# Performance work log

Hardware: AMD Instinct MI355X
Metric: run time of the kernel (lower is better)

## Reference

```python
import jax, jax.numpy as jnp
import numpy as np

BATCH = 1024
N_KPS = 24
N_IN = 6
N_HID = 128
N_OUT = 2
N_EDGES = N_KPS * (N_KPS - 1)  # 552, fully-connected minus self-loops
BN_EPS = 1e-5


def _xavier(key, shape):
    # torch xavier_normal_: std = sqrt(2 / (fan_in + fan_out)); Linear weight is [out, in]
    std = np.sqrt(2.0 / (shape[0] + shape[1])).astype(np.float32)
    return jax.random.normal(key, shape, dtype=jnp.float32) * std


def _mlp(x, w1, b1, w2, b2, g, be):
    # Two-layer ELU MLP followed by training-mode BatchNorm1d over flattened (B*N, C)
    h = jax.nn.elu(jnp.einsum('bnd,hd->bnh', x, w1) + b1)
    h = jax.nn.elu(jnp.einsum('bnd,hd->bnh', h, w2) + b2)
    mean = h.mean(axis=(0, 1))
    var = h.var(axis=(0, 1))  # biased variance, as torch BN uses for normalization
    return g * (h - mean) * jax.lax.rsqrt(var + BN_EPS) + be


def setup_inputs() -> dict:
    key = jax.random.key(0)
    ks = jax.random.split(key, 12)
    # structural one-hot receiver/sender matrices for fully-connected graph (no self-loops)
    off = ~np.eye(N_KPS, dtype=bool)
    recv_idx, send_idx = np.nonzero(off)
    eye = np.eye(N_KPS, dtype=np.float32)
    rel_rec = jnp.asarray(eye[recv_idx])    # [E, N]
    rel_send = jnp.asarray(eye[send_idx])   # [E, N]

    inputs = jax.random.normal(ks[0], (BATCH, N_KPS, N_IN), dtype=jnp.float32)

    def mlp_params(k, n_in):
        k1, k2 = jax.random.split(k)
        return dict(
            w1=_xavier(k1, (N_HID, n_in)), b1=jnp.full((N_HID,), 0.1, jnp.float32),
            w2=_xavier(k2, (N_HID, N_HID)), b2=jnp.full((N_HID,), 0.1, jnp.float32),
            g=jnp.ones((N_HID,), jnp.float32), be=jnp.zeros((N_HID,), jnp.float32))

    m1 = mlp_params(ks[1], N_IN)
    m2 = mlp_params(ks[2], 2 * N_HID)
    m3 = mlp_params(ks[3], N_HID)
    m4 = mlp_params(ks[4], 3 * N_HID)
    fo_w = _xavier(ks[5], (N_OUT, N_HID * N_KPS))
    fo_b = jnp.full((N_OUT,), 0.1, jnp.float32)

    d = {'inputs': inputs, 'rel_rec': rel_rec, 'rel_send': rel_send,
         'fo_w': fo_w, 'fo_b': fo_b}
    for name, p in [('m1', m1), ('m2', m2), ('m3', m3), ('m4', m4)]:
        for k2, v in p.items():
            d[f'{name}_{k2}'] = v
    return d


def reference(inputs, rel_rec, rel_send,
              fo_w, fo_b,
              m1_w1, m1_b1, m1_w2, m1_b2, m1_g, m1_be,
              m2_w1, m2_b1, m2_w2, m2_b2, m2_g, m2_be,
              m3_w1, m3_b1, m3_w2, m3_b2, m3_g, m3_be,
              m4_w1, m4_b1, m4_w2, m4_b2, m4_g, m4_be):
    B, N = inputs.shape[0], inputs.shape[1]
    x = inputs.reshape(B, N, -1)

    def node2edge(x):  # [B,N,C] -> [B,E,2C]
        recv = jnp.einsum('en,bnc->bec', rel_rec, x)
        send = jnp.einsum('en,bnc->bec', rel_send, x)
        return jnp.concatenate([recv, send], axis=2)

    def edge2node(x):  # [B,E,C] -> [B,N,C], averaged by N (= incoming.size(1))
        return jnp.einsum('en,bec->bnc', rel_rec, x) / N

    x = _mlp(x, m1_w1, m1_b1, m1_w2, m1_b2, m1_g, m1_be)            # [B,N,H]
    x = _mlp(node2edge(x), m2_w1, m2_b1, m2_w2, m2_b2, m2_g, m2_be)  # [B,E,H]
    x_skip = x
    x = _mlp(edge2node(x), m3_w1, m3_b1, m3_w2, m3_b2, m3_g, m3_be)  # [B,N,H]
    x = node2edge(x)                                                  # [B,E,2H]
    x = jnp.concatenate([x, x_skip], axis=2)                          # [B,E,3H]
    x = _mlp(x, m4_w1, m4_b1, m4_w2, m4_b2, m4_g, m4_be)              # [B,E,H]
    x = edge2node(x)                                                  # [B,N,H]
    x = x.reshape(B, -1)                                              # [B,N*H]
    return x @ fo_w.T + fo_b                                          # [B,n_out]
```

## Files before the change

### kernel.cpp

```cpp
#include <hip/hip_runtime.h>

typedef __bf16 bf16;
typedef __bf16 b16x8 __attribute__((ext_vector_type(8)));
typedef __bf16 b16x4 __attribute__((ext_vector_type(4)));
typedef float f32x4 __attribute__((ext_vector_type(4)));

#define TB 256
#define LDA 136
#define LDI 40
#define NB 1024
#define NK 24
#define NE 552
#define NH 128
#define BEcnt (NB*NE)
#define BNODE (NB*NK)
#define EPS 1e-5f

#define S_BN1 0
#define S_BN3 2048
#define S_A2  4096
#define S_A4  20480
#define S_B41 36864
#define STATS_ZERO_BYTES 147456
#define WB_M1W2 0
#define WB_M2W1 16384
#define WB_M2W2 49152
#define WB_M3W1 65536
#define WB_M3W2 81920
#define WB_M4W1 98304
#define WB_M4W2 147456
#define WB_M4W1S 163840
#define OFF_WBF 150528ull
#define OFF_H1  516096ull
#define OFF_H3  (OFF_H1 + 6291456ull)
#define OFF_Y2R (OFF_H3 + 6291456ull)
#define OFF_Y2S (OFF_Y2R + 6291456ull)
#define OFF_Y4R (OFF_Y2S + 6291456ull)
#define OFF_Y4S (OFF_Y4R + 6291456ull)
#define OFF_Z2  (OFF_Y4S + 6291456ull)
#define OFF_Z4  (OFF_Z2  + 12582912ull)
#define OFF_H2  (OFF_Z4  + 12582912ull)

__device__ __forceinline__ float elu(float x){ return x > 0.f ? x : __expf(x) - 1.f; }

__device__ __forceinline__ void swizzle_bt(int id, int& b, int& tile4){
  int x = id & 7, j = id >> 3;
  int bt = j / 6;
  int tile = j - bt*6;
  b = x*128 + bt;
  tile4 = tile*4;
}

__device__ __forceinline__ void load_bfrags_bf(const bf16* W, int ldw, int k0,
                                               b16x8 bfr[4][2], int lane, int w){
  int n = lane & 15, q = lane >> 4;
  #pragma unroll
  for (int kb=0; kb<4; ++kb)
    #pragma unroll
    for (int t=0; t<2; ++t)
      bfr[kb][t] = *(const b16x8*)(W + (size_t)((w*2+t)*16 + n)*ldw + k0 + kb*32 + q*8);
}

template<int MT>
__device__ __forceinline__ void gemm_regB_t(const bf16* As, const b16x8 bfr[4][2],
                                            f32x4 acc[MT][2], int lane){
  int m = lane & 15, q = lane >> 4;
  #pragma unroll
  for (int kb=0; kb<4; ++kb){
    int ka = kb*32 + q*8;
    b16x8 a[MT];
    #pragma unroll
    for (int mt=0; mt<MT; ++mt)
      a[mt] = *(const b16x8*)(As + (mt*16+m)*LDA + ka);
    #pragma unroll
    for (int mt=0; mt<MT; ++mt)
      #pragma unroll
      for (int t=0; t<2; ++t)
        acc[mt][t] = __builtin_amdgcn_mfma_f32_16x16x32_bf16(a[mt], bfr[kb][t], acc[mt][t], 0,0,0);
  }
}

template<int MT>
__device__ __forceinline__ void zero_acc_t(f32x4 acc[MT][2]){
  #pragma unroll
  for (int mt=0; mt<MT; ++mt)
    #pragma unroll
    for (int t=0; t<2; ++t){ acc[mt][t][0]=0.f; acc[mt][t][1]=0.f; acc[mt][t][2]=0.f; acc[mt][t][3]=0.f; }
}

template<int MT>
__device__ __forceinline__ void epilogue_to_lds_t(const f32x4 acc[MT][2], const float* bias, bf16* As,
                                                  int lane, int w, int validRows){
  int q = lane >> 4, n = lane & 15;
  #pragma unroll
  for (int mt=0; mt<MT; ++mt)
    #pragma unroll
    for (int t=0; t<2; ++t){
      int col = (w*2+t)*16 + n;
      float bc = bias[col];
      #pragma unroll
      for (int i=0; i<4; ++i){
        int row = mt*16 + q*4 + i;
        float v = (row < validRows) ? elu(acc[mt][t][i] + bc) : 0.f;
        As[row*LDA + col] = (bf16)v;
      }
    }
}

template<int MT>
__device__ __forceinline__ void write_acc_bf_t(const f32x4 acc[MT][2], bf16* out, int lane, int w){
  int q = lane >> 4, n = lane & 15;
  #pragma unroll
  for (int mt=0; mt<MT; ++mt)
    #pragma unroll
    for (int t=0; t<2; ++t){
      int col = (w*2+t)*16 + n;
      #pragma unroll
      for (int i=0; i<4; ++i)
        out[(size_t)(mt*16 + q*4 + i)*NH + col] = (bf16)acc[mt][t][i];
    }
}

__device__ __forceinline__ void store_and_stats32(const bf16* As, bf16* g_out, float* bucket,
                                                  int tid){
  for (int i = tid; i < 32*16; i += TB){
    int row = i >> 4, c8 = (i & 15) << 3;
    *(b16x8*)(g_out + (size_t)row*NH + c8) = *(const b16x8*)(As + row*LDA + c8);
  }
  int c = tid & 127, half = tid >> 7;
  float s = 0.f, s2 = 0.f;
  for (int row = half; row < 32; row += 2){
    float v = (float)As[row*LDA + c];
    s += v; s2 += v*v;
  }
  atomicAdd(&bucket[c], s);
  atomicAdd(&bucket[128+c], s2);
}

__device__ __forceinline__ void build_A_g(bf16* As, const bf16* yrG, const bf16* ysG,
                                          const float* bias, int tile4, int tid){
  for (int i=tid; i<96*16; i+=TB){
    int row = i >> 4, c8 = (i & 15) << 3;
    b16x8 o;
    if (row < 92){
      int rl = (row>=23)+(row>=46)+(row>=69);
      int j = row - rl*23;
      int s = j + (j >= tile4 + rl);
      b16x8 vr = *(const b16x8*)(yrG + (size_t)rl*NH + c8);
      b16x8 vs = *(const b16x8*)(ysG + (size_t)s*NH + c8);
      #pragma unroll
      for (int k=0; k<8; ++k) o[k] = (bf16)elu((float)vr[k] + (float)vs[k] + bias[c8+k]);
    } else {
      #pragma unroll
      for (int k=0; k<8; ++k) o[k] = (bf16)0.f;
    }
    *(b16x8*)(As + row*LDA + c8) = o;
  }
}

__device__ __forceinline__ void harvest_core(const f32x4 acc[6][2], const float* bias, bf16* As,
                                             float* zL, float* sacc, int lane, int w){
  int q4 = (lane >> 4) << 2, n = lane & 15;
  int c0 = w*32 + n, c1 = c0 + 16;
  float b0 = bias[c0], b1 = bias[c1];
  float zs0[4] = {0,0,0,0}, zs1[4] = {0,0,0,0};
  float s0=0.f, p0=0.f, s1=0.f, p1=0.f;
  #pragma unroll
  for (int mt=0; mt<6; ++mt){
    #pragma unroll
    for (int i=0; i<4; ++i){
      const int R0 = mt*16 + i;
      int row = R0 + q4;
      bool ok = row < 92;
      float v0 = elu(acc[mt][0][i] + b0); v0 = ok ? v0 : 0.f;
      float v1 = elu(acc[mt][1][i] + b1); v1 = ok ? v1 : 0.f;
      if (As){
        As[row*LDA + c0] = (bf16)v0;
        As[row*LDA + c1] = (bf16)v1;
      }
      s0 += v0; p0 += v0*v0; s1 += v1; p1 += v1*v1;
      const int gLo = (R0>=23)+(R0>=46)+(R0>=69);
      const int gHi = ((R0+12)>=23)+((R0+12)>=46)+((R0+12)>=69);
      if (gLo == gHi){
        zs0[gLo] += v0; zs1[gLo] += v1;
      } else {
        const int bnd = (gHi==1) ? 23 : ((gHi==2) ? 46 : 69);
        bool hi = row >= bnd;
        zs0[gLo] += hi ? 0.f : v0;  zs0[gHi] += hi ? v0 : 0.f;
        zs1[gLo] += hi ? 0.f : v1;  zs1[gHi] += hi ? v1 : 0.f;
      }
    }
  }
  #pragma unroll
  for (int g=0; g<4; ++g){
    zs0[g] += __shfl_down(zs0[g],32); zs0[g] += __shfl_down(zs0[g],16);
    zs1[g] += __shfl_down(zs1[g],32); zs1[g] += __shfl_down(zs1[g],16);
  }
  s0 += __shfl_down(s0,32); s0 += __shfl_down(s0,16);
  p0 += __shfl_down(p0,32); p0 += __shfl_down(p0,16);
  s1 += __shfl_down(s1,32); s1 += __shfl_down(s1,16);
  p1 += __shfl_down(p1,32); p1 += __shfl_down(p1,16);
  if (lane < 16){
    #pragma unroll
    for (int g=0; g<4; ++g){
      zL[g*NH + c0] = zs0[g];
      zL[g*NH + c1] = zs1[g];
    }
    atomicAdd(&sacc[c0], s0);     atomicAdd(&sacc[128+c0], p0);
    atomicAdd(&sacc[c1], s1);     atomicAdd(&sacc[128+c1], p1);
  }
}

__global__ __launch_bounds__(TB) void k0_cvt(const float* __restrict__ s0, const float* __restrict__ s1,
    const float* __restrict__ s2, const float* __restrict__ s3, const float* __restrict__ s4,
    const float* __restrict__ s5, const float* __restrict__ s6, bf16* __restrict__ dst){
  int idx = (blockIdx.x*TB + threadIdx.x)*4;
  const float* sp; int base;
  if      (idx < 16384){ sp=s0; base=0; }
  else if (idx < 49152){ sp=s1; base=16384; }
  else if (idx < 65536){ sp=s2; base=49152; }
  else if (idx < 81920){ sp=s3; base=65536; }
  else if (idx < 98304){ sp=s4; base=81920; }
  else if (idx <147456){ sp=s5; base=98304; }
  else                 { sp=s6; base=147456; }
  f32x4 v = *(const f32x4*)(sp + (idx - base));
  b16x4 o; o[0]=(bf16)v[0]; o[1]=(bf16)v[1]; o[2]=(bf16)v[2]; o[3]=(bf16)v[3];
  *(b16x4*)(dst + idx) = o;
}

__global__ __launch_bounds__(TB) void k_fold41(const float* __restrict__ w41, const float* __restrict__ b41,
    const float* __restrict__ A2, const float* __restrict__ g2, const float* __restrict__ be2,
    bf16* __restrict__ w41s, float* __restrict__ b41f){
  __shared__ float tmp[256], scl[128], shf[128];
  int tid = threadIdx.x;
  { int c = tid & 127, part = tid >> 7;
    float s = 0.f;
    for (int r=0; r<64; ++r) s += A2[r*256 + part*128 + c];
    tmp[tid] = s; }
  __syncthreads();
  if (tid < 128){
    float mean = tmp[tid] / (float)BEcnt;
    float var  = tmp[128+tid] / (float)BEcnt - mean*mean;
    float sc = g2[tid] * rsqrtf(var + EPS);
    scl[tid] = sc; shf[tid] = be2[tid] - mean*sc;
  }
  __syncthreads();
  if (blockIdx.x < 16){
    int idx = (blockIdx.x*TB + tid)*4;
    int o = idx >> 7, k = idx & 127;
    f32x4 v = *(const f32x4*)(w41 + (size_t)o*384 + 256 + k);
    b16x4 r;
    #pragma unroll
    for (int j=0; j<4; ++j) r[j] = (bf16)(v[j] * scl[k+j]);
    *(b16x4*)(w41s + idx) = r;
  } else if (tid < 128){
    const float* wr = w41 + (size_t)tid*384 + 256;
    float s = 0.f;
    for (int k=0; k<128; ++k) s += wr[k] * shf[k];
    b41f[tid] = b41[tid] + s;
  }
}

__global__ __launch_bounds__(TB) void k1_mlp1(const float* __restrict__ in,
    const float* __restrict__ w1, const float* __restrict__ b1,
    const bf16* __restrict__ w2, const float* __restrict__ b2,
    bf16* __restrict__ h1, float* __restrict__ bn1){
  __shared__ alignas(16) bf16 As[32*LDA];
  __shared__ float w1s[128*6];
  __shared__ float b1s[128], b2s[128];
  __shared__ float ins[32*6];
  int tid = threadIdx.x;
  int row0 = blockIdx.x * 32;
  for (int i=tid; i<768; i+=TB) w1s[i] = w1[i];
  if (tid < 128){ b1s[tid]=b1[tid]; b2s[tid]=b2[tid]; }
  for (int i=tid; i<192; i+=TB) ins[i] = in[row0*6 + i];
  __syncthreads();
  for (int i=tid; i<32*32; i+=TB){
    int row = i >> 5, c4 = (i & 31) << 2;
    float x0=ins[row*6+0], x1=ins[row*6+1], x2=ins[row*6+2],
          x3=ins[row*6+3], x4=ins[row*6+4], x5=ins[row*6+5];
    #pragma unroll
    for (int j=0; j<4; ++j){
      int c = c4 + j;
      const float* wr = w1s + c*6;
      float s = b1s[c] + wr[0]*x0 + wr[1]*x1 + wr[2]*x2 + wr[3]*x3 + wr[4]*x4 + wr[5]*x5;
      As[row*LDA + c] = (bf16)elu(s);
    }
  }
  int lane = tid & 63, w = tid >> 6;
  b16x8 bfr[4][2];
  load_bfrags_bf(w2, 128, 0, bfr, lane, w);
  __syncthreads();
  f32x4 acc[2][2]; zero_acc_t<2>(acc);
  gemm_regB_t<2>(As, bfr, acc, lane);
  __syncthreads();
  epilogue_to_lds_t<2>(acc, b2s, As, lane, w, 32);
  __syncthreads();
  store_and_stats32(As, h1 + (size_t)row0*NH, bn1 + (blockIdx.x & 7)*256, tid);
}

__global__ __launch_bounds__(TB) void k_project(const bf16* __restrict__ hin,
    const float* __restrict__ stats,
    const float* __restrict__ g, const float* __restrict__ be,
    const bf16* __restrict__ Wp, int ldw,
    bf16* __restrict__ yr, bf16* __restrict__ ys){
  __shared__ alignas(16) bf16 As[32*LDA];
  __shared__ float scl[128], shf[128];
  int tid = threadIdx.x;
  int row0 = blockIdx.x * 32;
  if (tid < 128){
    float s = 0.f, q2 = 0.f;
    #pragma unroll
    for (int k=0; k<8; ++k){ s += stats[k*256+tid]; q2 += stats[k*256+128+tid]; }
    float mean = s / (float)BNODE;
    float var  = q2 / (float)BNODE - mean*mean;
    float rs = rsqrtf(var + EPS);
    float sc = g[tid] * rs;
    scl[tid] = sc; shf[tid] = be[tid] - mean*sc;
  }
  __syncthreads();
  for (int i=tid; i<32*16; i+=TB){
    int row = i >> 4, c8 = (i & 15) << 3;
    b16x8 v = *(const b16x8*)(hin + (size_t)(row0+row)*NH + c8);
    b16x8 o;
    #pragma unroll
    for (int j=0; j<8; ++j) o[j] = (bf16)(scl[c8+j]*(float)v[j] + shf[c8+j]);
    *(b16x8*)(As + row*LDA + c8) = o;
  }
  int lane = tid & 63, w = tid >> 6;
  b16x8 bfr[4][2];
  load_bfrags_bf(Wp, ldw, 0, bfr, lane, w);
  __syncthreads();
  f32x4 acc[2][2]; zero_acc_t<2>(acc);
  gemm_regB_t<2>(As, bfr, acc, lane);
  write_acc_bf_t<2>(acc, yr + (size_t)row0*NH, lane, w);
  load_bfrags_bf(Wp, ldw, 128, bfr, lane, w);
  zero_acc_t<2>(acc);
  gemm_regB_t<2>(As, bfr, acc, lane);
  write_acc_bf_t<2>(acc, ys + (size_t)row0*NH, lane, w);
}

__global__ __launch_bounds__(TB,4) void k3_edge1(const bf16* __restrict__ y2r, const bf16* __restrict__ y2s,
    const float* __restrict__ b21, const bf16* __restrict__ w22, const float* __restrict__ b22,
    float* __restrict__ z2, float* __restrict__ acc2, bf16* __restrict__ h2){
  __shared__ alignas(16) bf16 As[96*LDA];
  __shared__ float b1s[NH], b2s[NH];
  __shared__ float zL[512];
  int tid = threadIdx.x;
  int b, tile4; swizzle_bt(blockIdx.x, b, tile4);
  if (tid < NH){ b1s[tid]=b21[tid]; b2s[tid]=b22[tid]; }
  int lane = tid & 63, w = tid >> 6;
  b16x8 bfr[4][2];
  load_bfrags_bf(w22, 128, 0, bfr, lane, w);
  __syncthreads();
  build_A_g(As, y2r + ((size_t)b*NK + tile4)*NH, y2s + (size_t)b*NK*NH, b1s, tile4, tid);
  __syncthreads();
  f32x4 acc[6][2]; zero_acc_t<6>(acc);
  gemm_regB_t<6>(As, bfr, acc, lane);
  __syncthreads();
  harvest_core(acc, b2s, As, zL, acc2 + (blockIdx.x & 63)*256, lane, w);
  __syncthreads();
  float* zdst = z2 + (size_t)(b*NK + tile4)*NH;
  if (tid < 128) ((f32x4*)zdst)[tid] = ((const f32x4*)zL)[tid];
  bf16* h2g = h2 + ((size_t)b*NE + tile4*23)*NH;
  for (int i=tid; i<92*16; i+=TB){
    int row = i >> 4, c8 = (i & 15) << 3;
    *(b16x8*)(h2g + (size_t)row*NH + c8) = *(const b16x8*)(As + row*LDA + c8);
  }
}

__global__ __launch_bounds__(TB) void k4a_mlp3(const float* __restrict__ z2,
    const float* __restrict__ A2,
    const float* __restrict__ g2, const float* __restrict__ be2,
    const bf16* __restrict__ w31, const float* __restrict__ b31,
    const bf16* __restrict__ w32, const float* __restrict__ b32,
    bf16* __restrict__ h3, float* __restrict__ bn3){
  __shared__ alignas(16) bf16 As[32*LDA];
  __shared__ float scl[128], shf[128], b1s[128], b2s[128];
  __shared__ float tmp[256];
  int tid = threadIdx.x;
  int row0 = blockIdx.x * 32;
  { int c = tid & 127, part = tid >> 7;
    float s = 0.f;
    for (int r=0; r<64; ++r) s += A2[r*256 + part*128 + c];
    tmp[tid] = s; }
  if (tid < 128){ b1s[tid] = b31[tid]; b2s[tid] = b32[tid]; }
  __syncthreads();
  if (tid < 128){
    float mean = tmp[tid] / (float)BEcnt;
    float var  = tmp[128+tid] / (float)BEcnt - mean*mean;
    float sc = g2[tid] * rsqrtf(var + EPS);
    scl[tid] = sc * (1.f/24.f);
    shf[tid] = (be2[tid] - mean*sc) * (23.f/24.f);
  }
  __syncthreads();
  for (int i=tid; i<32*32; i+=TB){
    int rl = i >> 5, c4 = (i & 31) << 2;
    f32x4 v = *(const f32x4*)(z2 + (size_t)(row0+rl)*NH + c4);
    b16x4 o;
    #pragma unroll
    for (int k=0; k<4; ++k) o[k] = (bf16)(scl[c4+k]*v[k] + shf[c4+k]);
    *(b16x4*)(As + rl*LDA + c4) = o;
  }
  int lane = tid & 63, w = tid >> 6;
  b16x8 bfr[4][2];
  load_bfrags_bf(w31, 128, 0, bfr, lane, w);
  __syncthreads();
  f32x4 acc[2][2]; zero_acc_t<2>(acc);
  gemm_regB_t<2>(As, bfr, acc, lane);
  __syncthreads();
  epilogue_to_lds_t<2>(acc, b1s, As, lane, w, 32);
  load_bfrags_bf(w32, 128, 0, bfr, lane, w);
  __syncthreads();
  zero_acc_t<2>(acc);
  gemm_regB_t<2>(As, bfr, acc, lane);
  __syncthreads();
  epilogue_to_lds_t<2>(acc, b2s, As, lane, w, 32);
  __syncthreads();
  store_and_stats32(As, h3 + (size_t)row0*NH, bn3 + (blockIdx.x & 7)*256, tid);
}

__global__ __launch_bounds__(TB,3) void k5_edge2(
    const bf16* __restrict__ h2,
    const bf16* __restrict__ y4r, const bf16* __restrict__ y4s,
    const bf16* __restrict__ w41s, const float* __restrict__ b41f,
    const bf16* __restrict__ w42, const float* __restrict__ b42,
    float* __restrict__ z4, float* __restrict__ acc4){
  __shared__ alignas(16) bf16 As[96*LDA];
  __shared__ alignas(16) bf16 Ai[96*LDI];
  __shared__ float b42s[NH];
  __shared__ float zL[512];
  int tid = threadIdx.x;
  int b, tile4; swizzle_bt(blockIdx.x, b, tile4);
  if (tid < NH) b42s[tid] = b42[tid];
  int lane = tid & 63, w = tid >> 6;
  b16x8 bfr[4][2];
  load_bfrags_bf(w41s, 128, 0, bfr, lane, w);
  b16x8 baug[2];
  {
    const bf16* y4rG = y4r + ((size_t)b*NK + tile4)*NH;
    const bf16* y4sG = y4s + (size_t)b*NK*NH;
    int q = lane >> 4, n = lane & 15;
    #pragma unroll
    for (int t=0; t<2; ++t){
      int o = w*32 + t*16 + n;
      #pragma unroll
      for (int j=0; j<8; ++j){
        int k = q*8 + j;
        bf16 v;
        if (k < 4)        v = y4rG[(size_t)k*NH + o];
        else if (k < 28)  v = y4sG[(size_t)(k-4)*NH + o];
        else if (k == 28) v = (bf16)b41f[o];
        else              v = (bf16)0.f;
        baug[t][j] = v;
      }
    }
  }
  for (int i=tid; i<96*4; i+=TB){
    int row = i >> 2, cb = (i & 3) << 3;
    int rl = (row>=23)+(row>=46)+(row>=69);
    int jj = row - rl*23;
    int s = jj + (jj >= tile4 + rl);
    b16x8 o;
    #pragma unroll
    for (int k2=0; k2<8; ++k2){
      int k = cb + k2;
      bool one = (row < 92) && (k == rl || k == 4+s || k == 28);
      o[k2] = one ? (bf16)1.f : (bf16)0.f;
    }
    *(b16x8*)(Ai + row*LDI + cb) = o;
  }
  {
    const bf16* h2g = h2 + ((size_t)b*NE + tile4*23)*NH;
    for (int i=tid; i<96*16; i+=TB){
      int row = i >> 4, c8 = (i & 15) << 3;
      b16x8 o;
      if (row < 92){
        o = *(const b16x8*)(h2g + (size_t)row*NH + c8);
      } else {
        #pragma unroll
        for (int j=0; j<8; ++j) o[j] = (bf16)0.f;
      }
      *(b16x8*)(As + row*LDA + c8) = o;
    }
  }
  __syncthreads();
  f32x4 acc[6][2]; zero_acc_t<6>(acc);
  gemm_regB_t<6>(As, bfr, acc, lane);
  {
    int m = lane & 15, q = lane >> 4;
    #pragma unroll
    for (int mt=0; mt<6; ++mt){
      b16x8 a = *(const b16x8*)(Ai + (mt*16+m)*LDI + q*8);
      #pragma unroll
      for (int t=0; t<2; ++t)
        acc[mt][t] = __builtin_amdgcn_mfma_f32_16x16x32_bf16(a, baug[t], acc[mt][t], 0,0,0);
    }
  }
  load_bfrags_bf(w42, 128, 0, bfr, lane, w);
  __syncthreads();
  {
    int q = lane >> 4, n = lane & 15;
    #pragma unroll
    for (int mt=0; mt<6; ++mt)
      #pragma unroll
      for (int t=0; t<2; ++t){
        int col = w*32 + t*16 + n;
        #pragma unroll
        for (int i=0; i<4; ++i)
          As[(mt*16 + q*4 + i)*LDA + col] = (bf16)elu(acc[mt][t][i]);
      }
  }
  zero_acc_t<6>(acc);
  __syncthreads();
  gemm_regB_t<6>(As, bfr, acc, lane);
  harvest_core(acc, b42s, nullptr, zL, acc4 + (blockIdx.x & 63)*256, lane, w);
  __syncthreads();
  float* zdst = z4 + (size_t)(b*NK + tile4)*NH;
  if (tid < 128) ((f32x4*)zdst)[tid] = ((const f32x4*)zL)[tid];
}

__global__ __launch_bounds__(TB) void k6_out(const float* __restrict__ z4,
    const float* __restrict__ A4,
    const float* __restrict__ g4, const float* __restrict__ be4,
    const float* __restrict__ fo_w, const float* __restrict__ fo_b, float* __restrict__ out){
  __shared__ float red[512];
  __shared__ float scl[128], shf[128];
  int tid = threadIdx.x, b = blockIdx.x;
  { int c = tid & 127, part = tid >> 7;
    float s = 0.f;
    for (int r=0; r<64; ++r) s += A4[r*256 + part*128 + c];
    red[tid] = s; }
  __syncthreads();
  if (tid < 128){
    float mean = red[tid] / (float)BEcnt;
    float var  = red[128+tid] / (float)BEcnt - mean*mean;
    float sc = g4[tid] * rsqrtf(var + EPS);
    scl[tid] = sc; shf[tid] = be4[tid] - mean*sc;
  }
  __syncthreads();
  const float inv24 = 1.f/24.f, f2324 = 23.f/24.f;
  float a0 = 0.f, a1 = 0.f;
  for (int i=tid; i<3072; i+=TB){
    int c = i & 127;
    float x = scl[c]*z4[(size_t)b*3072 + i]*inv24 + shf[c]*f2324;
    a0 += x * fo_w[i];
    a1 += x * fo_w[3072 + i];
  }
  __syncthreads();
  red[tid] = a0; red[256+tid] = a1;
  __syncthreads();
  for (int st=128; st>0; st>>=1){
    if (tid < st){ red[tid] += red[tid+st]; red[256+tid] += red[256+tid+st]; }
    __syncthreads();
  }
  if (tid == 0){
    out[b*2+0] = red[0] + fo_b[0];
    out[b*2+1] = red[256] + fo_b[1];
  }
}

extern "C" void kernel_launch(void* const* d_in, const int* in_sizes, int n_in,
                              void* d_out, int out_size, void* d_ws, size_t ws_size,
                              hipStream_t stream){
  (void)in_sizes; (void)n_in; (void)out_size; (void)ws_size;
  const float* inputs = (const float*)d_in[0];
  const float* fo_w  = (const float*)d_in[3];
  const float* fo_b  = (const float*)d_in[4];
  const float* m1_w1=(const float*)d_in[5];  const float* m1_b1=(const float*)d_in[6];
  const float* m1_w2=(const float*)d_in[7];  const float* m1_b2=(const float*)d_in[8];
  const float* m1_g =(const float*)d_in[9];  const float* m1_be=(const float*)d_in[10];
  const float* m2_w1=(const float*)d_in[11]; const float* m2_b1=(const float*)d_in[12];
  const float* m2_w2=(const float*)d_in[13]; const float* m2_b2=(const float*)d_in[14];
  const float* m2_g =(const float*)d_in[15]; const float* m2_be=(const float*)d_in[16];
  const float* m3_w1=(const float*)d_in[17]; const float* m3_b1=(const float*)d_in[18];
  const float* m3_w2=(const float*)d_in[19]; const float* m3_b2=(const float*)d_in[20];
  const float* m3_g =(const float*)d_in[21]; const float* m3_be=(const float*)d_in[22];
  const float* m4_w1=(const float*)d_in[23]; const float* m4_b1=(const float*)d_in[24];
  const float* m4_w2=(const float*)d_in[25]; const float* m4_b2=(const float*)d_in[26];
  const float* m4_g =(const float*)d_in[27]; const float* m4_be=(const float*)d_in[28];

  char* ws = (char*)d_ws;
  float* stats = (float*)ws;
  bf16* wbf = (bf16*)(ws + OFF_WBF);
  bf16* h1  = (bf16*)(ws + OFF_H1);
  bf16* h3  = (bf16*)(ws + OFF_H3);
  bf16* y2r = (bf16*)(ws + OFF_Y2R);
  bf16* y2s = (bf16*)(ws + OFF_Y2S);
  bf16* y4r = (bf16*)(ws + OFF_Y4R);
  bf16* y4s = (bf16*)(ws + OFF_Y4S);
  float* z2  = (float*)(ws + OFF_Z2);
  float* z4  = (float*)(ws + OFF_Z4);
  bf16* h2  = (bf16*)(ws + OFF_H2);
  float* out = (float*)d_out;

  (void)hipMemsetAsync(d_ws, 0, STATS_ZERO_BYTES, stream);
  k0_cvt<<<160, TB, 0, stream>>>(m1_w2, m2_w1, m2_w2, m3_w1, m3_w2, m4_w1, m4_w2, wbf);
  k1_mlp1<<<768, TB, 0, stream>>>(inputs, m1_w1, m1_b1, wbf + WB_M1W2, m1_b2, h1, stats + S_BN1);
  k_project<<<768, TB, 0, stream>>>(h1, stats + S_BN1, m1_g, m1_be,
                                    wbf + WB_M2W1, 256, y2r, y2s);
  k3_edge1<<<6144, TB, 0, stream>>>(y2r, y2s, m2_b1, wbf + WB_M2W2, m2_b2, z2,
                                    stats + S_A2, h2);
  k_fold41<<<17, TB, 0, stream>>>(m4_w1, m4_b1, stats + S_A2, m2_g, m2_be,
                                  wbf + WB_M4W1S, stats + S_B41);
  k4a_mlp3<<<768, TB, 0, stream>>>(z2, stats + S_A2, m2_g, m2_be,
                                   wbf + WB_M3W1, m3_b1, wbf + WB_M3W2, m3_b2,
                                   h3, stats + S_BN3);
  k_project<<<768, TB, 0, stream>>>(h3, stats + S_BN3, m3_g, m3_be,
                                    wbf + WB_M4W1, 384, y4r, y4s);
  k5_edge2<<<6144, TB, 0, stream>>>(h2, y4r, y4s,
                                    wbf + WB_M4W1S, stats + S_B41,
                                    wbf + WB_M4W2, m4_b2, z4, stats + S_A4);
  k6_out<<<1024, TB, 0, stream>>>(z4, stats + S_A4, m4_g, m4_be, fo_w, fo_b, out);
}
```

Measured before the change: 323.0 us.

## Make edge kernels persistent per batch, looping over six tiles per block

The two edge kernels launch one block per batch element instead of one per (batch, tile) pair and loop over the six receiver tiles inside the block. This lets weight fragments loaded into registers be reused across tiles and, in the first edge kernel, stages the sender projections in shared memory once per batch. It cuts grid size from 6144 to 1024 blocks, which reduces parallelism and latency hiding. It also adds extra block-wide barriers per tile, and in the second kernel the second weight load now repeats every tile.

```diff
diff --git a/kernel.cpp b/kernel.cpp
--- a/kernel.cpp
+++ b/kernel.cpp
@@ -43,14 +43,6 @@
 
 __device__ __forceinline__ float elu(float x){ return x > 0.f ? x : __expf(x) - 1.f; }
 
-__device__ __forceinline__ void swizzle_bt(int id, int& b, int& tile4){
-  int x = id & 7, j = id >> 3;
-  int bt = j / 6;
-  int tile = j - bt*6;
-  b = x*128 + bt;
-  tile4 = tile*4;
-}
-
 __device__ __forceinline__ void load_bfrags_bf(const bf16* W, int ldw, int k0,
                                                b16x8 bfr[4][2], int lane, int w){
   int n = lane & 15, q = lane >> 4;
@@ -135,27 +127,6 @@
   }
   atomicAdd(&bucket[c], s);
   atomicAdd(&bucket[128+c], s2);
-}
-
-__device__ __forceinline__ void build_A_g(bf16* As, const bf16* yrG, const bf16* ysG,
-                                          const float* bias, int tile4, int tid){
-  for (int i=tid; i<96*16; i+=TB){
-    int row = i >> 4, c8 = (i & 15) << 3;
-    b16x8 o;
-    if (row < 92){
-      int rl = (row>=23)+(row>=46)+(row>=69);
-      int j = row - rl*23;
-      int s = j + (j >= tile4 + rl);
-      b16x8 vr = *(const b16x8*)(yrG + (size_t)rl*NH + c8);
-      b16x8 vs = *(const b16x8*)(ysG + (size_t)s*NH + c8);
-      #pragma unroll
-      for (int k=0; k<8; ++k) o[k] = (bf16)elu((float)vr[k] + (float)vs[k] + bias[c8+k]);
-    } else {
-      #pragma unroll
-      for (int k=0; k<8; ++k) o[k] = (bf16)0.f;
-    }
-    *(b16x8*)(As + row*LDA + c8) = o;
-  }
 }
 
 __device__ __forceinline__ void harvest_core(const f32x4 acc[6][2], const float* bias, bf16* As,
@@ -344,28 +315,58 @@
     const float* __restrict__ b21, const bf16* __restrict__ w22, const float* __restrict__ b22,
     float* __restrict__ z2, float* __restrict__ acc2, bf16* __restrict__ h2){
   __shared__ alignas(16) bf16 As[96*LDA];
+  __shared__ alignas(16) bf16 yts[24*LDA];
   __shared__ float b1s[NH], b2s[NH];
   __shared__ float zL[512];
   int tid = threadIdx.x;
-  int b, tile4; swizzle_bt(blockIdx.x, b, tile4);
+  int x = blockIdx.x & 7, bt = blockIdx.x >> 3;
+  int b = x*128 + bt;
   if (tid < NH){ b1s[tid]=b21[tid]; b2s[tid]=b22[tid]; }
+  {
+    const bf16* ysB = y2s + (size_t)b*NK*NH;
+    for (int i=tid; i<24*16; i+=TB){
+      int r = i >> 4, c8 = (i & 15) << 3;
+      *(b16x8*)(yts + r*LDA + c8) = *(const b16x8*)(ysB + (size_t)r*NH + c8);
+    }
+  }
   int lane = tid & 63, w = tid >> 6;
   b16x8 bfr[4][2];
   load_bfrags_bf(w22, 128, 0, bfr, lane, w);
   __syncthreads();
-  build_A_g(As, y2r + ((size_t)b*NK + tile4)*NH, y2s + (size_t)b*NK*NH, b1s, tile4, tid);
-  __syncthreads();
-  f32x4 acc[6][2]; zero_acc_t<6>(acc);
-  gemm_regB_t<6>(As, bfr, acc, lane);
-  __syncthreads();
-  harvest_core(acc, b2s, As, zL, acc2 + (blockIdx.x & 63)*256, lane, w);
-  __syncthreads();
-  float* zdst = z2 + (size_t)(b*NK + tile4)*NH;
-  if (tid < 128) ((f32x4*)zdst)[tid] = ((const f32x4*)zL)[tid];
-  bf16* h2g = h2 + ((size_t)b*NE + tile4*23)*NH;
-  for (int i=tid; i<92*16; i+=TB){
-    int row = i >> 4, c8 = (i & 15) << 3;
-    *(b16x8*)(h2g + (size_t)row*NH + c8) = *(const b16x8*)(As + row*LDA + c8);
+  for (int tile=0; tile<6; ++tile){
+    int tile4 = tile*4;
+    const bf16* yrG = y2r + ((size_t)b*NK + tile4)*NH;
+    for (int i=tid; i<96*16; i+=TB){
+      int row = i >> 4, c8 = (i & 15) << 3;
+      b16x8 o;
+      if (row < 92){
+        int rl = (row>=23)+(row>=46)+(row>=69);
+        int j = row - rl*23;
+        int s = j + (j >= tile4 + rl);
+        b16x8 vr = *(const b16x8*)(yrG + (size_t)rl*NH + c8);
+        b16x8 vs = *(const b16x8*)(yts + s*LDA + c8);
+        #pragma unroll
+        for (int k=0; k<8; ++k) o[k] = (bf16)elu((float)vr[k] + (float)vs[k] + b1s[c8+k]);
+      } else {
+        #pragma unroll
+        for (int k=0; k<8; ++k) o[k] = (bf16)0.f;
+      }
+      *(b16x8*)(As + row*LDA + c8) = o;
+    }
+    __syncthreads();
+    f32x4 acc[6][2]; zero_acc_t<6>(acc);
+    gemm_regB_t<6>(As, bfr, acc, lane);
+    __syncthreads();
+    harvest_core(acc, b2s, As, zL, acc2 + (blockIdx.x & 63)*256, lane, w);
+    __syncthreads();
+    float* zdst = z2 + (size_t)(b*NK + tile4)*NH;
+    if (tid < 128) ((f32x4*)zdst)[tid] = ((const f32x4*)zL)[tid];
+    bf16* h2g = h2 + ((size_t)b*NE + tile4*23)*NH;
+    for (int i=tid; i<92*16; i+=TB){
+      int row = i >> 4, c8 = (i & 15) << 3;
+      *(b16x8*)(h2g + (size_t)row*NH + c8) = *(const b16x8*)(As + row*LDA + c8);
+    }
+    __syncthreads();
   }
 }
 
@@ -431,15 +432,15 @@
   __shared__ float b42s[NH];
   __shared__ float zL[512];
   int tid = threadIdx.x;
-  int b, tile4; swizzle_bt(blockIdx.x, b, tile4);
+  int x = blockIdx.x & 7, bt = blockIdx.x >> 3;
+  int b = x*128 + bt;
   if (tid < NH) b42s[tid] = b42[tid];
   int lane = tid & 63, w = tid >> 6;
-  b16x8 bfr[4][2];
-  load_bfrags_bf(w41s, 128, 0, bfr, lane, w);
+  b16x8 bfr1[4][2];
+  load_bfrags_bf(w41s, 128, 0, bfr1, lane, w);
   b16x8 baug[2];
+  const bf16* y4sG = y4s + (size_t)b*NK*NH;
   {
-    const bf16* y4rG = y4r + ((size_t)b*NK + tile4)*NH;
-    const bf16* y4sG = y4s + (size_t)b*NK*NH;
     int q = lane >> 4, n = lane & 15;
     #pragma unroll
     for (int t=0; t<2; ++t){
@@ -448,76 +449,93 @@
       for (int j=0; j<8; ++j){
         int k = q*8 + j;
         bf16 v;
-        if (k < 4)        v = y4rG[(size_t)k*NH + o];
-        else if (k < 28)  v = y4sG[(size_t)(k-4)*NH + o];
-        else if (k == 28) v = (bf16)b41f[o];
-        else              v = (bf16)0.f;
+        if (k >= 4 && k < 28)  v = y4sG[(size_t)(k-4)*NH + o];
+        else if (k == 28)      v = (bf16)b41f[o];
+        else                   v = (bf16)0.f;
         baug[t][j] = v;
       }
     }
   }
-  for (int i=tid; i<96*4; i+=TB){
-    int row = i >> 2, cb = (i & 3) << 3;
-    int rl = (row>=23)+(row>=46)+(row>=69);
-    int jj = row - rl*23;
-    int s = jj + (jj >= tile4 + rl);
-    b16x8 o;
-    #pragma unroll
-    for (int k2=0; k2<8; ++k2){
-      int k = cb + k2;
-      bool one = (row < 92) && (k == rl || k == 4+s || k == 28);
-      o[k2] = one ? (bf16)1.f : (bf16)0.f;
-    }
-    *(b16x8*)(Ai + row*LDI + cb) = o;
-  }
-  {
-    const bf16* h2g = h2 + ((size_t)b*NE + tile4*23)*NH;
-    for (int i=tid; i<96*16; i+=TB){
-      int row = i >> 4, c8 = (i & 15) << 3;
+  for (int tile=0; tile<6; ++tile){
+    int tile4 = tile*4;
+    {
+      const bf16* y4rG = y4r + ((size_t)b*NK + tile4)*NH;
+      int q = lane >> 4, n = lane & 15;
+      if (q == 0){
+        #pragma unroll
+        for (int t=0; t<2; ++t){
+          int o = w*32 + t*16 + n;
+          #pragma unroll
+          for (int j=0; j<4; ++j)
+            baug[t][j] = y4rG[(size_t)j*NH + o];
+        }
+      }
+    }
+    for (int i=tid; i<96*4; i+=TB){
+      int row = i >> 2, cb = (i & 3) << 3;
+      int rl = (row>=23)+(row>=46)+(row>=69);
+      int jj = row - rl*23;
+      int s = jj + (jj >= tile4 + rl);
       b16x8 o;
-      if (row < 92){
-        o = *(const b16x8*)(h2g + (size_t)row*NH + c8);
-      } else {
+      #pragma unroll
+      for (int k2=0; k2<8; ++k2){
+        int k = cb + k2;
+        bool one = (row < 92) && (k == rl || k == 4+s || k == 28);
+        o[k2] = one ? (bf16)1.f : (bf16)0.f;
+      }
+      *(b16x8*)(Ai + row*LDI + cb) = o;
+    }
+    {
+      const bf16* h2g = h2 + ((size_t)b*NE + tile4*23)*NH;
+      for (int i=tid; i<96*16; i+=TB){
+        int row = i >> 4, c8 = (i & 15) << 3;
+        b16x8 o;
+        if (row < 92){
+          o = *(const b16x8*)(h2g + (size_t)row*NH + c8);
+        } else {
+          #pragma unroll
+          for (int j=0; j<8; ++j) o[j] = (bf16)0.f;
+        }
+        *(b16x8*)(As + row*LDA + c8) = o;
+      }
+    }
+    __syncthreads();
+    f32x4 acc[6][2]; zero_acc_t<6>(acc);
+    gemm_regB_t<6>(As, bfr1, acc, lane);
+    {
+      int m = lane & 15, q = lane >> 4;
+      #pragma unroll
+      for (int mt=0; mt<6; ++mt){
+        b16x8 a = *(const b16x8*)(Ai + (mt*16+m)*LDI + q*8);
         #pragma unroll
-        for (int j=0; j<8; ++j) o[j] = (bf16)0.f;
-      }
-      *(b16x8*)(As + row*LDA + c8) = o;
-    }
-  }
-  __syncthreads();
-  f32x4 acc[6][2]; zero_acc_t<6>(acc);
-  gemm_regB_t<6>(As, bfr, acc, lane);
-  {
-    int m = lane & 15, q = lane >> 4;
-    #pragma unroll
-    for (int mt=0; mt<6; ++mt){
-      b16x8 a = *(const b16x8*)(Ai + (mt*16+m)*LDI + q*8);
+        for (int t=0; t<2; ++t)
+          acc[mt][t] = __builtin_amdgcn_mfma_f32_16x16x32_bf16(a, baug[t], acc[mt][t], 0,0,0);
+      }
+    }
+    b16x8 bfr2[4][2];
+    load_bfrags_bf(w42, 128, 0, bfr2, lane, w);
+    __syncthreads();
+    {
+      int q = lane >> 4, n = lane & 15;
       #pragma unroll
-      for (int t=0; t<2; ++t)
-        acc[mt][t] = __builtin_amdgcn_mfma_f32_16x16x32_bf16(a, baug[t], acc[mt][t], 0,0,0);
-    }
-  }
-  load_bfrags_bf(w42, 128, 0, bfr, lane, w);
-  __syncthreads();
-  {
-    int q = lane >> 4, n = lane & 15;
-    #pragma unroll
-    for (int mt=0; mt<6; ++mt)
-      #pragma unroll
-      for (int t=0; t<2; ++t){
-        int col = w*32 + t*16 + n;
+      for (int mt=0; mt<6; ++mt)
         #pragma unroll
-        for (int i=0; i<4; ++i)
-          As[(mt*16 + q*4 + i)*LDA + col] = (bf16)elu(acc[mt][t][i]);
-      }
-  }
-  zero_acc_t<6>(acc);
-  __syncthreads();
-  gemm_regB_t<6>(As, bfr, acc, lane);
-  harvest_core(acc, b42s, nullptr, zL, acc4 + (blockIdx.x & 63)*256, lane, w);
-  __syncthreads();
-  float* zdst = z4 + (size_t)(b*NK + tile4)*NH;
-  if (tid < 128) ((f32x4*)zdst)[tid] = ((const f32x4*)zL)[tid];
+        for (int t=0; t<2; ++t){
+          int col = w*32 + t*16 + n;
+          #pragma unroll
+          for (int i=0; i<4; ++i)
+            As[(mt*16 + q*4 + i)*LDA + col] = (bf16)elu(acc[mt][t][i]);
+        }
+    }
+    zero_acc_t<6>(acc);
+    __syncthreads();
+    gemm_regB_t<6>(As, bfr2, acc, lane);
+    harvest_core(acc, b42s, nullptr, zL, acc4 + (blockIdx.x & 63)*256, lane, w);
+    __syncthreads();
+    float* zdst = z4 + (size_t)(b*NK + tile4)*NH;
+    if (tid < 128) ((f32x4*)zdst)[tid] = ((const f32x4*)zL)[tid];
+    __syncthreads();
+  }
 }
 
 __global__ __launch_bounds__(TB) void k6_out(const float* __restrict__ z4,
@@ -599,7 +617,7 @@
   k1_mlp1<<<768, TB, 0, stream>>>(inputs, m1_w1, m1_b1, wbf + WB_M1W2, m1_b2, h1, stats + S_BN1);
   k_project<<<768, TB, 0, stream>>>(h1, stats + S_BN1, m1_g, m1_be,
                                     wbf + WB_M2W1, 256, y2r, y2s);
-  k3_edge1<<<6144, TB, 0, stream>>>(y2r, y2s, m2_b1, wbf + WB_M2W2, m2_b2, z2,
+  k3_edge1<<<1024, TB, 0, stream>>>(y2r, y2s, m2_b1, wbf + WB_M2W2, m2_b2, z2,
                                     stats + S_A2, h2);
   k_fold41<<<17, TB, 0, stream>>>(m4_w1, m4_b1, stats + S_A2, m2_g, m2_be,
                                   wbf + WB_M4W1S, stats + S_B41);
@@ -608,7 +626,7 @@
                                    h3, stats + S_BN3);
   k_project<<<768, TB, 0, stream>>>(h3, stats + S_BN3, m3_g, m3_be,
                                     wbf + WB_M4W1, 384, y4r, y4s);
-  k5_edge2<<<6144, TB, 0, stream>>>(h2, y4r, y4s,
+  k5_edge2<<<1024, TB, 0, stream>>>(h2, y4r, y4s,
                                     wbf + WB_M4W1S, stats + S_B41,
                                     wbf + WB_M4W2, m4_b2, z4, stats + S_A4);
   k6_out<<<1024, TB, 0, stream>>>(z4, stats + S_A4, m4_g, m4_be, fo_w, fo_b, out);
```

Result: slower. 353.2 us (+9.3%).
